# Kernel tuning notes

Measured on AMD Instinct MI355X. Metric: run time of the kernel, lower is better.

## Reference

```python
import jax, jax.numpy as jnp
import numpy as np

DIM = 192
HEADS = 6
WS = 7          # window size
SS = 3          # shift size
MLP_H = int(DIM * 4.0)
EPS_LN = 1e-5


def _static_tables():
    # Swin-v2 log-spaced continuous relative coords table: (1, 2*WS-1, 2*WS-1, 2)
    ch = np.arange(-(WS - 1), WS, dtype=np.float32)
    cw = np.arange(-(WS - 1), WS, dtype=np.float32)
    t = np.stack(np.meshgrid(ch, cw, indexing='ij'), axis=-1)[None]
    t[..., 0] /= (WS - 1)
    t[..., 1] /= (WS - 1)
    t *= 7.0
    t = np.sign(t) * np.log2(np.abs(t) + 1.0) / np.log2(7.0)
    # relative position index: (WS*WS, WS*WS)
    coords = np.stack(np.meshgrid(np.arange(WS), np.arange(WS), indexing='ij'))
    cf = coords.reshape(2, -1)
    rc = (cf[:, :, None] - cf[:, None, :]).transpose(1, 2, 0)
    rc[..., 0] += WS - 1
    rc[..., 1] += WS - 1
    rc[..., 0] *= 2 * WS - 1
    rpi = rc.sum(-1)
    return jnp.asarray(t, jnp.float32), jnp.asarray(rpi, jnp.int32)


def _attn_mask(H, W):
    # shifted-window mask: (nW, N, N) with 0 / -100
    img = np.zeros((H, W), np.float32)
    cnt = 0
    for hs in (slice(0, -WS), slice(-WS, -SS), slice(-SS, None)):
        for ws in (slice(0, -WS), slice(-WS, -SS), slice(-SS, None)):
            img[hs, ws] = cnt
            cnt += 1
    mw = img.reshape(H // WS, WS, W // WS, WS).transpose(0, 2, 1, 3).reshape(-1, WS * WS)
    am = mw[:, None, :] - mw[:, :, None]
    am = np.where(am != 0, -100.0, 0.0).astype(np.float32)
    return jnp.asarray(am)


def _ln(x, w, b):
    m = x.mean(-1, keepdims=True)
    v = ((x - m) ** 2).mean(-1, keepdims=True)
    return (x - m) / jnp.sqrt(v + EPS_LN) * w + b


def setup_inputs() -> dict:
    key = jax.random.key(0)
    ks = jax.random.split(key, 16)
    d = DIM
    inp = {
        'x': jax.random.normal(ks[0], (32, 56, 56, d), jnp.float32),
        'qkv_w': jax.random.normal(ks[1], (3 * d, d), jnp.float32) * (2.0 / d) ** 0.5,
        'qkv_b': jnp.full((3 * d,), 0.01, jnp.float32),
        'proj_w': jax.random.normal(ks[2], (d, d), jnp.float32) * (2.0 / d) ** 0.5,
        'proj_b': jnp.full((d,), 0.01, jnp.float32),
        'logit_scale': jnp.log(10.0 * jnp.ones((HEADS, 1, 1), jnp.float32)),
        'cpb_w1': jax.random.normal(ks[3], (512, 2), jnp.float32) * (2.0 / 2) ** 0.5,
        'cpb_b1': jnp.full((512,), 0.01, jnp.float32),
        'cpb_w2': jax.random.normal(ks[4], (HEADS, 512), jnp.float32) * (2.0 / 512) ** 0.5,
        'norm1_w': jnp.ones((d,), jnp.float32),
        'norm1_b': jnp.zeros((d,), jnp.float32),
        'norm2_w': jnp.ones((d,), jnp.float32),
        'norm2_b': jnp.zeros((d,), jnp.float32),
        'fc1_w': jax.random.normal(ks[5], (MLP_H, d), jnp.float32) * (2.0 / d) ** 0.5,
        'fc1_b': jnp.full((MLP_H,), 0.01, jnp.float32),
        'fc2_w': jax.random.normal(ks[6], (d, MLP_H), jnp.float32) * (2.0 / MLP_H) ** 0.5,
        'fc2_b': jnp.full((d,), 0.01, jnp.float32),
    }
    return inp


def reference(x, qkv_w, qkv_b, proj_w, proj_b, logit_scale, cpb_w1, cpb_b1, cpb_w2,
              norm1_w, norm1_b, norm2_w, norm2_b, fc1_w, fc1_b, fc2_w, fc2_b):
    B, H, W, C = x.shape
    N = WS * WS
    hd = C // HEADS
    table, rpi = _static_tables()
    mask = _attn_mask(H, W)  # (nW, N, N)
    nW = mask.shape[0]

    shortcut = x
    # cyclic shift + window partition: (B*nW, N, C)
    xs = jnp.roll(x, (-SS, -SS), axis=(1, 2))
    xw = xs.reshape(B, H // WS, WS, W // WS, WS, C).transpose(0, 1, 3, 2, 4, 5).reshape(-1, N, C)

    qkv = xw @ qkv_w.T + qkv_b
    qkv = qkv.reshape(-1, N, 3, HEADS, hd).transpose(2, 0, 3, 1, 4)
    q, k, v = qkv[0], qkv[1], qkv[2]  # (B_, H, N, hd)

    qn = q / jnp.clip(jnp.linalg.norm(q, axis=-1, keepdims=True), 1e-12)
    kn = k / jnp.clip(jnp.linalg.norm(k, axis=-1, keepdims=True), 1e-12)
    scale = jnp.exp(jnp.minimum(logit_scale, jnp.log(100.0)))  # (HEADS,1,1)
    attn = jnp.einsum('bhnd,bhmd->bhnm', qn, kn) * scale

    # CPB-MLP relative position bias
    hbt = jax.nn.leaky_relu(table @ cpb_w1.T + cpb_b1, 0.01) @ cpb_w2.T  # (1,13,13,HEADS)
    bias_table = hbt.reshape(-1, HEADS)
    rpb = bias_table[rpi.reshape(-1)].reshape(N, N, HEADS).transpose(2, 0, 1)
    attn = attn + (14.0 * jax.nn.sigmoid(rpb))[None]

    # shifted-window mask + softmax
    attn = attn.reshape(B, nW, HEADS, N, N) + mask[None, :, None]
    attn = jax.nn.softmax(attn.reshape(-1, HEADS, N, N), axis=-1)

    out = jnp.einsum('bhnm,bhmd->bnhd', attn, v).reshape(-1, N, C)
    out = out @ proj_w.T + proj_b

    # window reverse + reverse shift
    out = out.reshape(B, H // WS, W // WS, WS, WS, C).transpose(0, 1, 3, 2, 4, 5).reshape(B, H, W, C)
    out = jnp.roll(out, (SS, SS), axis=(1, 2))

    # post-norm residuals (Swin-v2 style)
    x1 = shortcut + _ln(out, norm1_w, norm1_b)
    mlp = jax.nn.gelu(x1 @ fc1_w.T + fc1_b, approximate=False) @ fc2_w.T + fc2_b
    return x1 + _ln(mlp, norm2_w, norm2_b)
```

## Files before the change

kernel.cpp:

```cpp
#include <hip/hip_runtime.h>
#include <math.h>

#define CDIM 192
#define NHEADS 6
#define HDIM 32
#define WSZ 7
#define NTOK 49
#define SHIFT 3
#define HW 56
#define MLPH 768
#define NTOKENS 100352
#define QKS 576
#define XS 200
#define VTS 72
#define PPS 72
#define LS 196
#define QPS 72
#define AS2 200
#define HS2 200
#define OS2 196

typedef __attribute__((ext_vector_type(8))) short short8;
typedef __attribute__((ext_vector_type(4))) float floatx4;
typedef unsigned short ushort_t;
typedef unsigned int uint_t;

__device__ __forceinline__ ushort_t f2b(float f) {
  __bf16 b = (__bf16)f;
  return __builtin_bit_cast(ushort_t, b);
}

__device__ __forceinline__ float gelu_fast(float v) {
  float u2 = 1.5957691f * v * (1.0f + 0.044715f * v * v);
  float s = 1.0f / (1.0f + __expf(-u2));
  return v * s;
}

__global__ void prep_kernel(const float* __restrict__ fc1_w, const float* __restrict__ fc2_w,
                            const float* __restrict__ qkv_w, const float* __restrict__ proj_w,
                            ushort_t* __restrict__ w1b, ushort_t* __restrict__ w2b,
                            ushort_t* __restrict__ qwb, ushort_t* __restrict__ pwb) {
  int i = blockIdx.x * 256 + threadIdx.x;
  if (i < MLPH*CDIM) w1b[i] = f2b(fc1_w[i]);
  else if (i < 2*MLPH*CDIM) w2b[i - MLPH*CDIM] = f2b(fc2_w[i - MLPH*CDIM]);
  else if (i < 2*MLPH*CDIM + 3*CDIM*CDIM) qwb[i - 2*MLPH*CDIM] = f2b(qkv_w[i - 2*MLPH*CDIM]);
  else if (i < 2*MLPH*CDIM + 4*CDIM*CDIM) {
    int j = i - 2*MLPH*CDIM - 3*CDIM*CDIM;
    int n = j / CDIM, k = j % CDIM;
    int h = k / 32, kloc = k % 32;
    int pos = (kloc < 16) ? 2*kloc : 2*(kloc-16) + 1;
    pwb[n*CDIM + h*32 + pos] = f2b(proj_w[j]);
  }
}

__global__ __launch_bounds__(256) void cpb1_kernel(const float* __restrict__ w1,
                                                   const float* __restrict__ b1,
                                                   const float* __restrict__ w2,
                                                   float* __restrict__ bt) {
  int wave = threadIdx.x >> 6, lane = threadIdx.x & 63;
  int e = blockIdx.x * 4 + wave;
  if (e >= 169) return;
  const float inv_log2_7 = 0.35620718710802217f;
  int a = e / 13, b = e % 13;
  float v0 = (float)(a - 6) * (7.0f / 6.0f);
  float v1 = (float)(b - 6) * (7.0f / 6.0f);
  float s0 = (v0 > 0.f) ? 1.f : ((v0 < 0.f) ? -1.f : 0.f);
  float s1 = (v1 > 0.f) ? 1.f : ((v1 < 0.f) ? -1.f : 0.f);
  v0 = s0 * log2f(fabsf(v0) + 1.0f) * inv_log2_7;
  v1 = s1 * log2f(fabsf(v1) + 1.0f) * inv_log2_7;
  float acc[NHEADS];
  #pragma unroll
  for (int h = 0; h < NHEADS; ++h) acc[h] = 0.f;
  #pragma unroll
  for (int j = 0; j < 8; ++j) {
    int k = lane + 64*j;
    float hv = v0 * w1[2*k] + v1 * w1[2*k+1] + b1[k];
    hv = (hv > 0.f) ? hv : 0.01f * hv;
    #pragma unroll
    for (int h = 0; h < NHEADS; ++h) acc[h] += hv * w2[h*512 + k];
  }
  #pragma unroll
  for (int m = 1; m < 64; m <<= 1)
    #pragma unroll
    for (int h = 0; h < NHEADS; ++h) acc[h] += __shfl_xor(acc[h], m, 64);
  if (lane == 0) {
    #pragma unroll
    for (int h = 0; h < NHEADS; ++h) bt[e*NHEADS + h] = acc[h];
  }
}

__global__ void cpb2_kernel(const float* __restrict__ bt, float* __restrict__ cbias) {
  int e = blockIdx.x * 256 + threadIdx.x;
  if (e >= 4*NHEADS*NTOK*NTOK) return;
  int cls = e / (NHEADS*NTOK*NTOK);
  int rem = e % (NHEADS*NTOK*NTOK);
  int h = rem / (NTOK*NTOK);
  int r = rem % (NTOK*NTOK);
  int i = r / NTOK, j = r % NTOK;
  int idx = (i/7 - j/7 + 6) * 13 + (i%7 - j%7 + 6);
  float v = bt[idx*NHEADS + h];
  float b = 14.0f / (1.0f + __expf(-v));
  int clsh = cls >> 1, clsw = cls & 1;
  int ri = (clsh ? HW-WSZ : 0) + i/7, rj = (clsh ? HW-WSZ : 0) + j/7;
  int ci = (clsw ? HW-WSZ : 0) + i%7, cj = (clsw ? HW-WSZ : 0) + j%7;
  int hi = (ri < HW-WSZ) ? 0 : ((ri < HW-SHIFT) ? 1 : 2);
  int hj = (rj < HW-WSZ) ? 0 : ((rj < HW-SHIFT) ? 1 : 2);
  int wi = (ci < HW-WSZ) ? 0 : ((ci < HW-SHIFT) ? 1 : 2);
  int wj = (cj < HW-WSZ) ? 0 : ((cj < HW-SHIFT) ? 1 : 2);
  if ((hi*3 + wi) != (hj*3 + wj)) b -= 100.f;
  cbias[e] = b;
}

__global__ __launch_bounds__(384) void qkv_kernel(
    const float* __restrict__ x, const ushort_t* __restrict__ qwb,
    const float* __restrict__ qkv_b, ushort_t* __restrict__ qkvg) {
  __shared__ __align__(16) ushort_t s_a[64*AS2];
  int tid = threadIdx.x;
  int lane = tid & 63;
  int h = tid >> 6;
  int l15 = lane & 15, quad = lane >> 4;
  size_t tbase = (size_t)blockIdx.x * 64;

  for (int e = tid; e < 64*48; e += 384) {
    int t = e / 48, cc = (e % 48) * 4;
    float4 v = *(const float4*)(x + (tbase + t)*CDIM + cc);
    uint_t p0 = (uint_t)f2b(v.x) | ((uint_t)f2b(v.y) << 16);
    uint_t p1 = (uint_t)f2b(v.z) | ((uint_t)f2b(v.w) << 16);
    *(uint_t*)&s_a[t*AS2 + cc]     = p0;
    *(uint_t*)&s_a[t*AS2 + cc + 2] = p1;
  }
  __syncthreads();

  floatx4 acc[6][4];
  #pragma unroll
  for (int nt = 0; nt < 6; ++nt)
    #pragma unroll
    for (int mt = 0; mt < 4; ++mt) acc[nt][mt] = (floatx4){0.f,0.f,0.f,0.f};
  #pragma unroll
  for (int kt = 0; kt < 6; ++kt) {
    short8 a[4];
    #pragma unroll
    for (int mt = 0; mt < 4; ++mt)
      a[mt] = *(const short8*)&s_a[(mt*16 + l15)*AS2 + kt*32 + quad*8];
    #pragma unroll
    for (int nt = 0; nt < 6; ++nt) {
      int o = (nt >> 1)*CDIM + h*HDIM + (nt & 1)*16 + l15;
      short8 b = *(const short8*)&qwb[(size_t)o*CDIM + kt*32 + quad*8];
      #pragma unroll
      for (int mt = 0; mt < 4; ++mt)
        acc[nt][mt] = __builtin_amdgcn_mfma_f32_16x16x32_bf16(a[mt], b, acc[nt][mt], 0, 0, 0);
    }
  }
  #pragma unroll
  for (int w2 = 0; w2 < 2; ++w2) {
    float b0 = qkv_b[w2*CDIM + h*HDIM + l15];
    float b1 = qkv_b[w2*CDIM + h*HDIM + 16 + l15];
    #pragma unroll
    for (int mt = 0; mt < 4; ++mt) {
      float vv[2][4], ss[4];
      #pragma unroll
      for (int r = 0; r < 4; ++r) {
        float t0 = acc[w2*2][mt][r] + b0;
        float t1 = acc[w2*2+1][mt][r] + b1;
        vv[0][r] = t0; vv[1][r] = t1;
        ss[r] = t0*t0 + t1*t1;
      }
      #pragma unroll
      for (int m = 1; m < 16; m <<= 1)
        #pragma unroll
        for (int r = 0; r < 4; ++r) ss[r] += __shfl_xor(ss[r], m, 64);
      #pragma unroll
      for (int r = 0; r < 4; ++r) {
        float inv = 1.0f / fmaxf(sqrtf(ss[r]), 1e-12f);
        size_t tok = tbase + mt*16 + quad*4 + r;
        uint_t pk = (uint_t)f2b(vv[0][r] * inv) | ((uint_t)f2b(vv[1][r] * inv) << 16);
        *(uint_t*)&qkvg[tok*QKS + w2*CDIM + h*HDIM + 2*l15] = pk;
      }
    }
  }
  {
    float b0 = qkv_b[2*CDIM + h*HDIM + l15];
    float b1 = qkv_b[2*CDIM + h*HDIM + 16 + l15];
    #pragma unroll
    for (int mt = 0; mt < 4; ++mt)
      #pragma unroll
      for (int r = 0; r < 4; ++r) {
        size_t tok = tbase + mt*16 + quad*4 + r;
        uint_t pk = (uint_t)f2b(acc[4][mt][r] + b0) | ((uint_t)f2b(acc[5][mt][r] + b1) << 16);
        *(uint_t*)&qkvg[tok*QKS + 2*CDIM + h*HDIM + 2*l15] = pk;
      }
  }
}

__global__ __launch_bounds__(512, 4) void attn_kernel(
    const float* __restrict__ x, const ushort_t* __restrict__ qkvg,
    const ushort_t* __restrict__ pwb, const float* __restrict__ proj_b,
    const float* __restrict__ logit_scale, const float* __restrict__ cbias,
    const float* __restrict__ n1w, const float* __restrict__ n1b,
    float* __restrict__ outp) {
  __shared__ __align__(16) ushort_t sm[192*VTS + 128*PPS + 64*XS];
  ushort_t* s_vt = sm;
  ushort_t* s_P  = sm + 192*VTS;
  ushort_t* s_o  = s_P + 128*PPS;
  float*    s_ln = (float*)sm;
  __shared__ float s_mu[NTOK], s_rs[NTOK];

  int tid = threadIdx.x;
  int lane = tid & 63;
  int wave = tid >> 6;
  int wm = wave & 3, wh = wave >> 2;
  int l15 = lane & 15, quad = lane >> 4;
  int mrow0 = wm*16 + quad*4;
  int blk = blockIdx.x;
  int bimg = blk >> 6, wh_b = (blk >> 3) & 7, ww_b = blk & 7;
  int rbase = wh_b*WSZ, cbase = ww_b*WSZ;
  const float* cb = cbias +
      (size_t)(((wh_b == 7) ? 2 : 0) + ((ww_b == 7) ? 1 : 0)) * (NHEADS*NTOK*NTOK);

  int ti_a = wm*16 + l15; ti_a = (ti_a < NTOK) ? ti_a : (NTOK-1);
  int ra = rbase + ti_a/7 + SHIFT; ra -= (ra >= HW) ? HW : 0;
  int ca = cbase + ti_a%7 + SHIFT; ca -= (ca >= HW) ? HW : 0;
  uint_t qrow = (uint_t)((bimg*HW + ra)*HW + ca) * QKS;
  uint_t krow[4];
  #pragma unroll
  for (int nt = 0; nt < 4; ++nt) {
    int tn = nt*16 + l15; tn = (tn < NTOK) ? tn : (NTOK-1);
    int r = rbase + tn/7 + SHIFT; r -= (r >= HW) ? HW : 0;
    int c = cbase + tn%7 + SHIFT; c -= (c >= HW) ? HW : 0;
    krow[nt] = (uint_t)((bimg*HW + r)*HW + c) * QKS + CDIM;
  }
  short8 aq[3];
  #pragma unroll
  for (int hh = 0; hh < 3; ++hh)
    aq[hh] = *(const short8*)&qkvg[(size_t)qrow + (wh*3+hh)*HDIM + quad*8];

  for (int e = tid; e < 32*48; e += 512) {
    int tp = e & 31, dg = e >> 5;
    int t0 = 2*tp, t1 = t0 + 1;
    uint2 va = make_uint2(0u, 0u), vb = make_uint2(0u, 0u);
    if (t0 < NTOK) {
      int r = rbase + t0/7 + SHIFT; r -= (r >= HW) ? HW : 0;
      int c = cbase + t0%7 + SHIFT; c -= (c >= HW) ? HW : 0;
      va = *(const uint2*)&qkvg[((size_t)((bimg*HW + r)*HW + c))*QKS + 2*CDIM + dg*4];
    }
    if (t1 < NTOK) {
      int r = rbase + t1/7 + SHIFT; r -= (r >= HW) ? HW : 0;
      int c = cbase + t1%7 + SHIFT; c -= (c >= HW) ? HW : 0;
      vb = *(const uint2*)&qkvg[((size_t)((bimg*HW + r)*HW + c))*QKS + 2*CDIM + dg*4];
    }
    int d = dg*4;
    *(uint_t*)&s_vt[(d  )*VTS + t0] = (va.x & 0xFFFFu) | (vb.x << 16);
    *(uint_t*)&s_vt[(d+1)*VTS + t0] = (va.x >> 16) | (vb.x & 0xFFFF0000u);
    *(uint_t*)&s_vt[(d+2)*VTS + t0] = (va.y & 0xFFFFu) | (vb.y << 16);
    *(uint_t*)&s_vt[(d+3)*VTS + t0] = (va.y >> 16) | (vb.y & 0xFFFF0000u);
  }
  __syncthreads();

  ushort_t* sPh = s_P + wave*16*PPS;
  short8 bk[4];
  #pragma unroll
  for (int nt = 0; nt < 4; ++nt)
    bk[nt] = *(const short8*)&qkvg[(size_t)krow[nt] + (wh*3)*HDIM + quad*8];
  for (int hh = 0; hh < 3; ++hh) {
    int h = wh*3 + hh;
    floatx4 sv[4];
    __builtin_amdgcn_s_setprio(1);
    #pragma unroll
    for (int nt = 0; nt < 4; ++nt)
      sv[nt] = __builtin_amdgcn_mfma_f32_16x16x32_bf16(aq[hh], bk[nt], (floatx4){0.f,0.f,0.f,0.f}, 0, 0, 0);
    __builtin_amdgcn_s_setprio(0);
    if (hh < 2) {
      #pragma unroll
      for (int nt = 0; nt < 4; ++nt)
        bk[nt] = *(const short8*)&qkvg[(size_t)krow[nt] + (h+1)*HDIM + quad*8];
    }
    float sc = __expf(fminf(logit_scale[h], 4.6051702f));
    #pragma unroll
    for (int r = 0; r < 4; ++r) {
      int m_tok = mrow0 + r;
      int mi = (m_tok < NTOK) ? m_tok : (NTOK-1);
      float srow[4];
      float mx = -1e30f;
      #pragma unroll
      for (int nt = 0; nt < 4; ++nt) {
        int n = nt*16 + l15;
        int ni = (n < NTOK) ? n : (NTOK-1);
        float s = sv[nt][r]*sc + cb[(h*NTOK + mi)*NTOK + ni];
        if (n >= NTOK) s = -1e30f;
        srow[nt] = s;
        mx = fmaxf(mx, s);
      }
      #pragma unroll
      for (int m = 1; m < 16; m <<= 1) mx = fmaxf(mx, __shfl_xor(mx, m, 64));
      float p[4], sum = 0.f;
      #pragma unroll
      for (int nt = 0; nt < 4; ++nt) { p[nt] = __expf(srow[nt] - mx); sum += p[nt]; }
      #pragma unroll
      for (int m = 1; m < 16; m <<= 1) sum += __shfl_xor(sum, m, 64);
      float inv = 1.0f / sum;
      #pragma unroll
      for (int nt = 0; nt < 4; ++nt) {
        int n = nt*16 + l15;
        sPh[(quad*4 + r)*PPS + n] = (n < NTOK) ? f2b(p[nt]*inv) : (ushort_t)0;
      }
    }
    floatx4 ov[2];
    ov[0] = (floatx4){0.f,0.f,0.f,0.f}; ov[1] = (floatx4){0.f,0.f,0.f,0.f};
    __builtin_amdgcn_s_setprio(1);
    #pragma unroll
    for (int kt = 0; kt < 2; ++kt) {
      short8 ap = *(const short8*)&sPh[l15*PPS + kt*32 + quad*8];
      #pragma unroll
      for (int dt = 0; dt < 2; ++dt) {
        short8 bv = *(const short8*)&s_vt[(h*HDIM + dt*16 + l15)*VTS + kt*32 + quad*8];
        ov[dt] = __builtin_amdgcn_mfma_f32_16x16x32_bf16(ap, bv, ov[dt], 0, 0, 0);
      }
    }
    __builtin_amdgcn_s_setprio(0);
    #pragma unroll
    for (int dt = 0; dt < 2; ++dt)
      #pragma unroll
      for (int r = 0; r < 4; ++r)
        s_o[(mrow0 + r)*XS + h*HDIM + dt*16 + l15] = f2b(ov[dt][r]);
  }
  __syncthreads();

  short8 aof[6];
  #pragma unroll
  for (int kt = 0; kt < 6; ++kt)
    aof[kt] = *(const short8*)&s_o[(wm*16 + l15)*XS + kt*32 + quad*8];
  floatx4 pacc[6];
  #pragma unroll
  for (int j = 0; j < 6; ++j) pacc[j] = (floatx4){0.f,0.f,0.f,0.f};
  #pragma unroll
  for (int kt = 0; kt < 6; ++kt) {
    #pragma unroll
    for (int j = 0; j < 6; ++j) {
      int n = wh*96 + j*16 + l15;
      short8 b = *(const short8*)&pwb[(size_t)n*CDIM + kt*32 + quad*8];
      pacc[j] = __builtin_amdgcn_mfma_f32_16x16x32_bf16(aof[kt], b, pacc[j], 0, 0, 0);
    }
  }
  #pragma unroll
  for (int j = 0; j < 6; ++j) {
    int c = wh*96 + j*16 + l15;
    float pb = proj_b[c];
    #pragma unroll
    for (int r = 0; r < 4; ++r) {
      int m = mrow0 + r;
      if (m < NTOK) s_ln[m*LS + c] = pacc[j][r] + pb;
    }
  }
  __syncthreads();
  if (tid < 4*NTOK) {
    int row = tid >> 2, part = tid & 3;
    const float4* rp = (const float4*)(s_ln + row*LS) + part*12;
    float mu = 0.f;
    #pragma unroll
    for (int c = 0; c < 12; ++c) { float4 v = rp[c]; mu += v.x+v.y+v.z+v.w; }
    mu += __shfl_xor(mu, 1, 64);
    mu += __shfl_xor(mu, 2, 64);
    mu *= (1.0f/CDIM);
    float var = 0.f;
    #pragma unroll
    for (int c = 0; c < 12; ++c) {
      float4 v = rp[c];
      float a0=v.x-mu, a1=v.y-mu, a2=v.z-mu, a3=v.w-mu;
      var += a0*a0 + a1*a1 + a2*a2 + a3*a3;
    }
    var += __shfl_xor(var, 1, 64);
    var += __shfl_xor(var, 2, 64);
    var *= (1.0f/CDIM);
    if (part == 0) { s_mu[row] = mu; s_rs[row] = rsqrtf(var + 1e-5f); }
  }
  __syncthreads();
  for (int e = tid; e < NTOK*48; e += 512) {
    int ti = e / 48, cc = (e % 48) * 4;
    int r = (rbase + ti/WSZ + SHIFT) % HW;
    int cl = (cbase + ti%WSZ + SHIFT) % HW;
    size_t g = (((size_t)bimg*HW + r)*HW + cl)*CDIM + cc;
    float4 xv = *(const float4*)(x + g);
    float4 wv = *(const float4*)(n1w + cc);
    float4 bv = *(const float4*)(n1b + cc);
    float mu = s_mu[ti], rs = s_rs[ti];
    float4 o;
    o.x = xv.x + (s_ln[ti*LS+cc  ] - mu)*rs*wv.x + bv.x;
    o.y = xv.y + (s_ln[ti*LS+cc+1] - mu)*rs*wv.y + bv.y;
    o.z = xv.z + (s_ln[ti*LS+cc+2] - mu)*rs*wv.z + bv.z;
    o.w = xv.w + (s_ln[ti*LS+cc+3] - mu)*rs*wv.w + bv.w;
    *(float4*)(outp + g) = o;
  }
}

__global__ __launch_bounds__(512, 4) void attn_fused(
    const float* __restrict__ x, const ushort_t* __restrict__ qwb,
    const float* __restrict__ qkv_b, const ushort_t* __restrict__ pwb,
    const float* __restrict__ proj_b, const float* __restrict__ logit_scale,
    const float* __restrict__ cbias, const float* __restrict__ n1w,
    const float* __restrict__ n1b, float* __restrict__ outp) {
  __shared__ __align__(16) ushort_t sm[64*XS + 2*64*QPS + 64*VTS + 2*64*PPS];
  ushort_t* s_x  = sm;
  ushort_t* s_qn = s_x  + 64*XS;
  ushort_t* s_kn = s_qn + 64*QPS;
  ushort_t* s_vt = s_kn + 64*QPS;
  ushort_t* s_P  = s_vt + 64*VTS;
  ushort_t* s_o  = s_x;
  float*    s_ln = (float*)sm;
  __shared__ float s_mu[NTOK], s_rs[NTOK];

  int tid = threadIdx.x;
  int lane = tid & 63;
  int wave = tid >> 6;
  int wm = wave & 3, wh = wave >> 2;
  int l15 = lane & 15, quad = lane >> 4;
  int mrow0 = wm*16 + quad*4;
  int blk = blockIdx.x;
  int bimg = blk >> 6, wh_b = (blk >> 3) & 7, ww_b = blk & 7;
  const float* cb = cbias +
      (size_t)(((wh_b == 7) ? 2 : 0) + ((ww_b == 7) ? 1 : 0)) * (NHEADS*NTOK*NTOK);

  for (int e = tid; e < 64*48; e += 512) {
    int i = e / 48, cc = (e % 48) * 4;
    uint_t p0 = 0, p1 = 0;
    if (i < NTOK) {
      int r = (wh_b*WSZ + i/WSZ + SHIFT) % HW;
      int c = (ww_b*WSZ + i%WSZ + SHIFT) % HW;
      float4 v = *(const float4*)(x + (((size_t)bimg*HW + r)*HW + c)*CDIM + cc);
      p0 = (uint_t)f2b(v.x) | ((uint_t)f2b(v.y) << 16);
      p1 = (uint_t)f2b(v.z) | ((uint_t)f2b(v.w) << 16);
    }
    *(uint_t*)&s_x[i*XS + cc]     = p0;
    *(uint_t*)&s_x[i*XS + cc + 2] = p1;
  }
  __syncthreads();

  short8 axf[6];
  #pragma unroll
  for (int kt = 0; kt < 6; ++kt)
    axf[kt] = *(const short8*)&s_x[(wm*16 + l15)*XS + kt*32 + quad*8];

  for (int g = 0; g < 3; ++g) {
    int h = g*2 + wh;
    floatx4 acc[6];
    #pragma unroll
    for (int nt = 0; nt < 6; ++nt) acc[nt] = (floatx4){0.f,0.f,0.f,0.f};
    #pragma unroll
    for (int kt = 0; kt < 6; ++kt) {
      short8 a = axf[kt];
      #pragma unroll
      for (int nt = 0; nt < 6; ++nt) {
        int o = (nt >> 1)*CDIM + h*HDIM + (nt & 1)*16 + l15;
        short8 b = *(const short8*)&qwb[(size_t)o*CDIM + kt*32 + quad*8];
        acc[nt] = __builtin_amdgcn_mfma_f32_16x16x32_bf16(a, b, acc[nt], 0, 0, 0);
      }
    }
    #pragma unroll
    for (int w2 = 0; w2 < 2; ++w2) {
      float vv[2][4], ss[4];
      #pragma unroll
      for (int r = 0; r < 4; ++r) ss[r] = 0.f;
      #pragma unroll
      for (int dt = 0; dt < 2; ++dt) {
        float bias = qkv_b[w2*CDIM + h*HDIM + dt*16 + l15];
        #pragma unroll
        for (int r = 0; r < 4; ++r) {
          float t = acc[w2*2 + dt][r] + bias;
          vv[dt][r] = t; ss[r] += t*t;
        }
      }
      #pragma unroll
      for (int m = 1; m < 16; m <<= 1)
        #pragma unroll
        for (int r = 0; r < 4; ++r) ss[r] += __shfl_xor(ss[r], m, 64);
      ushort_t* dst = w2 ? s_kn : s_qn;
      #pragma unroll
      for (int r = 0; r < 4; ++r) {
        float inv = 1.0f / fmaxf(sqrtf(ss[r]), 1e-12f);
        #pragma unroll
        for (int dt = 0; dt < 2; ++dt)
          dst[(mrow0 + r)*QPS + wh*HDIM + dt*16 + l15] = f2b(vv[dt][r] * inv);
      }
    }
    #pragma unroll
    for (int dt = 0; dt < 2; ++dt) {
      float bias = qkv_b[2*CDIM + h*HDIM + dt*16 + l15];
      int d = wh*HDIM + 2*l15 + dt;
      #pragma unroll
      for (int rp = 0; rp < 2; ++rp) {
        uint_t pk = (uint_t)f2b(acc[4+dt][2*rp] + bias) |
                    ((uint_t)f2b(acc[4+dt][2*rp+1] + bias) << 16);
        *(uint_t*)&s_vt[d*VTS + mrow0 + 2*rp] = pk;
      }
    }
    __syncthreads();

    short8 aq = *(const short8*)&s_qn[(wm*16 + l15)*QPS + wh*HDIM + quad*8];
    floatx4 sv[4];
    #pragma unroll
    for (int nt = 0; nt < 4; ++nt) {
      short8 bk = *(const short8*)&s_kn[(nt*16 + l15)*QPS + wh*HDIM + quad*8];
      sv[nt] = __builtin_amdgcn_mfma_f32_16x16x32_bf16(aq, bk, (floatx4){0.f,0.f,0.f,0.f}, 0, 0, 0);
    }
    float sc = __expf(fminf(logit_scale[h], 4.6051702f));
    ushort_t* sPh = s_P + wh*64*PPS;
    #pragma unroll
    for (int r = 0; r < 4; ++r) {
      int m_tok = mrow0 + r;
      int mi = (m_tok < NTOK) ? m_tok : (NTOK-1);
      float srow[4];
      float mx = -1e30f;
      #pragma unroll
      for (int nt = 0; nt < 4; ++nt) {
        int n = nt*16 + l15;
        int ni = (n < NTOK) ? n : (NTOK-1);
        float s = sv[nt][r]*sc + cb[(h*NTOK + mi)*NTOK + ni];
        if (n >= NTOK) s = -1e30f;
        srow[nt] = s;
        mx = fmaxf(mx, s);
      }
      #pragma unroll
      for (int m = 1; m < 16; m <<= 1) mx = fmaxf(mx, __shfl_xor(mx, m, 64));
      float p[4], sum = 0.f;
      #pragma unroll
      for (int nt = 0; nt < 4; ++nt) { p[nt] = __expf(srow[nt] - mx); sum += p[nt]; }
      #pragma unroll
      for (int m = 1; m < 16; m <<= 1) sum += __shfl_xor(sum, m, 64);
      float inv = 1.0f / sum;
      #pragma unroll
      for (int nt = 0; nt < 4; ++nt) {
        int n = nt*16 + l15;
        sPh[(mrow0 + r)*PPS + n] = (n < NTOK) ? f2b(p[nt]*inv) : (ushort_t)0;
      }
    }
    floatx4 ov[2];
    ov[0] = (floatx4){0.f,0.f,0.f,0.f}; ov[1] = (floatx4){0.f,0.f,0.f,0.f};
    #pragma unroll
    for (int kt = 0; kt < 2; ++kt) {
      short8 ap = *(const short8*)&sPh[(wm*16 + l15)*PPS + kt*32 + quad*8];
      #pragma unroll
      for (int dt = 0; dt < 2; ++dt) {
        short8 bv = *(const short8*)&s_vt[(wh*HDIM + dt*16 + l15)*VTS + kt*32 + quad*8];
        ov[dt] = __builtin_amdgcn_mfma_f32_16x16x32_bf16(ap, bv, ov[dt], 0, 0, 0);
      }
    }
    #pragma unroll
    for (int dt = 0; dt < 2; ++dt)
      #pragma unroll
      for (int r = 0; r < 4; ++r)
        s_o[(mrow0 + r)*XS + h*HDIM + dt*16 + l15] = f2b(ov[dt][r]);
    __syncthreads();
  }

  short8 aof[6];
  #pragma unroll
  for (int kt = 0; kt < 6; ++kt)
    aof[kt] = *(const short8*)&s_o[(wm*16 + l15)*XS + kt*32 + quad*8];
  __syncthreads();
  floatx4 pacc[6];
  #pragma unroll
  for (int j = 0; j < 6; ++j) pacc[j] = (floatx4){0.f,0.f,0.f,0.f};
  #pragma unroll
  for (int kt = 0; kt < 6; ++kt) {
    #pragma unroll
    for (int j = 0; j < 6; ++j) {
      int n = wh*96 + j*16 + l15;
      short8 b = *(const short8*)&pwb[(size_t)n*CDIM + kt*32 + quad*8];
      pacc[j] = __builtin_amdgcn_mfma_f32_16x16x32_bf16(aof[kt], b, pacc[j], 0, 0, 0);
    }
  }
  #pragma unroll
  for (int j = 0; j < 6; ++j) {
    int c = wh*96 + j*16 + l15;
    float pb = proj_b[c];
    #pragma unroll
    for (int r = 0; r < 4; ++r) {
      int m = mrow0 + r;
      if (m < NTOK) s_ln[m*LS + c] = pacc[j][r] + pb;
    }
  }
  __syncthreads();
  if (tid < NTOK) {
    const float4* row = (const float4*)(s_ln + tid*LS);
    float mu = 0.f;
    #pragma unroll 8
    for (int c = 0; c < 48; ++c) { float4 v = row[c]; mu += v.x+v.y+v.z+v.w; }
    mu *= (1.0f/CDIM);
    float var = 0.f;
    #pragma unroll 8
    for (int c = 0; c < 48; ++c) {
      float4 v = row[c];
      float a0=v.x-mu, a1=v.y-mu, a2=v.z-mu, a3=v.w-mu;
      var += a0*a0 + a1*a1 + a2*a2 + a3*a3;
    }
    var *= (1.0f/CDIM);
    s_mu[tid] = mu; s_rs[tid] = rsqrtf(var + 1e-5f);
  }
  __syncthreads();
  for (int e = tid; e < NTOK*48; e += 512) {
    int ti = e / 48, cc = (e % 48) * 4;
    int r = (wh_b*WSZ + ti/WSZ + SHIFT) % HW;
    int cl = (ww_b*WSZ + ti%WSZ + SHIFT) % HW;
    size_t g = (((size_t)bimg*HW + r)*HW + cl)*CDIM + cc;
    float4 xv = *(const float4*)(x + g);
    float4 wv = *(const float4*)(n1w + cc);
    float4 bv = *(const float4*)(n1b + cc);
    float mu = s_mu[ti], rs = s_rs[ti];
    float4 o;
    o.x = xv.x + (s_ln[ti*LS+cc  ] - mu)*rs*wv.x + bv.x;
    o.y = xv.y + (s_ln[ti*LS+cc+1] - mu)*rs*wv.y + bv.y;
    o.z = xv.z + (s_ln[ti*LS+cc+2] - mu)*rs*wv.z + bv.z;
    o.w = xv.w + (s_ln[ti*LS+cc+3] - mu)*rs*wv.w + bv.w;
    *(float4*)(outp + g) = o;
  }
}

__global__ __launch_bounds__(256) void mlp_kernel(
    const ushort_t* __restrict__ w1b, const ushort_t* __restrict__ w2b,
    const float* __restrict__ fc1_b, const float* __restrict__ fc2_b,
    const float* __restrict__ n2w, const float* __restrict__ n2b,
    float* __restrict__ io) {
  __shared__ __align__(16) ushort_t sm2[64*AS2 + 2*64*HS2];
  ushort_t* s_a  = sm2;
  ushort_t* s_h0 = sm2 + 64*AS2;
  ushort_t* s_h1 = s_h0 + 64*HS2;
  float*    s_o  = (float*)sm2;
  __shared__ float s_mu[64], s_rs[64];

  int tid = threadIdx.x;
  int lane = tid & 63;
  int wave = tid >> 6;
  int l15 = lane & 15, quad = lane >> 4;
  size_t base = (size_t)blockIdx.x * (64*CDIM);

  for (int e = tid; e < 64*48; e += 256) {
    int t = e / 48, cc = (e % 48) * 4;
    float4 v = *(const float4*)(io + base + t*CDIM + cc);
    uint_t p0 = (uint_t)f2b(v.x) | ((uint_t)f2b(v.y) << 16);
    uint_t p1 = (uint_t)f2b(v.z) | ((uint_t)f2b(v.w) << 16);
    *(uint_t*)&s_a[t*AS2 + cc]     = p0;
    *(uint_t*)&s_a[t*AS2 + cc + 2] = p1;
  }
  __syncthreads();

  floatx4 oacc[12];
  #pragma unroll
  for (int t = 0; t < 12; ++t) oacc[t] = (floatx4){0.f,0.f,0.f,0.f};

  #pragma unroll
  for (int ch = 0; ch < 4; ++ch) {
    ushort_t* sh = (ch & 1) ? s_h1 : s_h0;
    floatx4 hacc[12];
    #pragma unroll
    for (int t = 0; t < 12; ++t) hacc[t] = (floatx4){0.f,0.f,0.f,0.f};
    #pragma unroll
    for (int kt = 0; kt < 6; ++kt) {
      short8 a[4];
      #pragma unroll
      for (int mt = 0; mt < 4; ++mt)
        a[mt] = *(const short8*)&s_a[(mt*16 + l15)*AS2 + kt*32 + quad*8];
      #pragma unroll
      for (int nt = 0; nt < 3; ++nt) {
        int n = ch*192 + wave*48 + nt*16 + l15;
        short8 b = *(const short8*)&w1b[(size_t)n*CDIM + kt*32 + quad*8];
        #pragma unroll
        for (int mt = 0; mt < 4; ++mt)
          hacc[nt*4+mt] = __builtin_amdgcn_mfma_f32_16x16x32_bf16(a[mt], b, hacc[nt*4+mt], 0, 0, 0);
      }
    }
    #pragma unroll
    for (int nt = 0; nt < 3; ++nt) {
      int n = ch*192 + wave*48 + nt*16 + l15;
      int cloc = wave*48 + nt*16 + l15;
      float bias = fc1_b[n];
      #pragma unroll
      for (int mt = 0; mt < 4; ++mt) {
        #pragma unroll
        for (int r = 0; r < 4; ++r) {
          float v = hacc[nt*4+mt][r] + bias;
          sh[(mt*16 + quad*4 + r)*HS2 + cloc] = f2b(gelu_fast(v));
        }
      }
    }
    __syncthreads();
    #pragma unroll
    for (int kt = 0; kt < 6; ++kt) {
      short8 a2[4];
      #pragma unroll
      for (int mt = 0; mt < 4; ++mt)
        a2[mt] = *(const short8*)&sh[(mt*16 + l15)*HS2 + kt*32 + quad*8];
      #pragma unroll
      for (int nt = 0; nt < 3; ++nt) {
        int n2 = wave*48 + nt*16 + l15;
        short8 b2 = *(const short8*)&w2b[(size_t)n2*MLPH + ch*192 + kt*32 + quad*8];
        #pragma unroll
        for (int mt = 0; mt < 4; ++mt)
          oacc[nt*4+mt] = __builtin_amdgcn_mfma_f32_16x16x32_bf16(a2[mt], b2, oacc[nt*4+mt], 0, 0, 0);
      }
    }
  }

  #pragma unroll
  for (int nt = 0; nt < 3; ++nt) {
    int c = wave*48 + nt*16 + l15;
    float bb = fc2_b[c];
    #pragma unroll
    for (int mt = 0; mt < 4; ++mt) {
      #pragma unroll
      for (int r = 0; r < 4; ++r)
        s_o[(mt*16 + quad*4 + r)*OS2 + c] = oacc[nt*4+mt][r] + bb;
    }
  }
  __syncthreads();
  {
    int row = tid >> 2, part = tid & 3;
    const float4* rp = (const float4*)(s_o + row*OS2) + part*12;
    float mu = 0.f;
    #pragma unroll
    for (int c = 0; c < 12; ++c) { float4 v = rp[c]; mu += v.x+v.y+v.z+v.w; }
    mu += __shfl_xor(mu, 1, 64);
    mu += __shfl_xor(mu, 2, 64);
    mu *= (1.0f/CDIM);
    float var = 0.f;
    #pragma unroll
    for (int c = 0; c < 12; ++c) {
      float4 v = rp[c];
      float a0=v.x-mu, a1=v.y-mu, a2=v.z-mu, a3=v.w-mu;
      var += a0*a0 + a1*a1 + a2*a2 + a3*a3;
    }
    var += __shfl_xor(var, 1, 64);
    var += __shfl_xor(var, 2, 64);
    var *= (1.0f/CDIM);
    if (part == 0) { s_mu[row] = mu; s_rs[row] = rsqrtf(var + 1e-5f); }
  }
  __syncthreads();
  for (int e = tid; e < 64*48; e += 256) {
    int t = e / 48, cc = (e % 48) * 4;
    float4 xv = *(const float4*)(io + base + t*CDIM + cc);
    float4 wv = *(const float4*)(n2w + cc);
    float4 bv = *(const float4*)(n2b + cc);
    float mu = s_mu[t], rs = s_rs[t];
    float4 o;
    o.x = xv.x + (s_o[t*OS2+cc  ] - mu)*rs*wv.x + bv.x;
    o.y = xv.y + (s_o[t*OS2+cc+1] - mu)*rs*wv.y + bv.y;
    o.z = xv.z + (s_o[t*OS2+cc+2] - mu)*rs*wv.z + bv.z;
    o.w = xv.w + (s_o[t*OS2+cc+3] - mu)*rs*wv.w + bv.w;
    *(float4*)(io + base + t*CDIM + cc) = o;
  }
}

extern "C" void kernel_launch(void* const* d_in, const int* in_sizes, int n_in,
                              void* d_out, int out_size, void* d_ws, size_t ws_size,
                              hipStream_t stream) {
  const float* x           = (const float*)d_in[0];
  const float* qkv_w       = (const float*)d_in[1];
  const float* qkv_b       = (const float*)d_in[2];
  const float* proj_w      = (const float*)d_in[3];
  const float* proj_b      = (const float*)d_in[4];
  const float* logit_scale = (const float*)d_in[5];
  const float* cpb_w1      = (const float*)d_in[6];
  const float* cpb_b1      = (const float*)d_in[7];
  const float* cpb_w2      = (const float*)d_in[8];
  const float* n1w         = (const float*)d_in[9];
  const float* n1b         = (const float*)d_in[10];
  const float* n2w         = (const float*)d_in[11];
  const float* n2b         = (const float*)d_in[12];
  const float* fc1_w       = (const float*)d_in[13];
  const float* fc1_b       = (const float*)d_in[14];
  const float* fc2_w       = (const float*)d_in[15];
  const float* fc2_b       = (const float*)d_in[16];
  float* out = (float*)d_out;

  ushort_t* w1b = (ushort_t*)d_ws;
  ushort_t* w2b = w1b + MLPH*CDIM;
  ushort_t* qwb = w2b + CDIM*MLPH;
  ushort_t* pwb = qwb + 3*CDIM*CDIM;
  float* cbias  = (float*)(pwb + CDIM*CDIM);
  float* bt     = cbias + 4*NHEADS*NTOK*NTOK;
  ushort_t* qkvg = (ushort_t*)(bt + 169*NHEADS);

  size_t base_b = (size_t)(2*MLPH*CDIM + 4*CDIM*CDIM)*2
                + (size_t)(4*NHEADS*NTOK*NTOK)*4 + (size_t)(169*NHEADS)*4;
  size_t qkvg_b = (size_t)NTOKENS*QKS*2;
  bool split_qkv = ws_size >= base_b + qkvg_b;

  int prep_elems = 2*MLPH*CDIM + 4*CDIM*CDIM;
  hipLaunchKernelGGL(prep_kernel, dim3((prep_elems + 255)/256), dim3(256), 0, stream,
                     fc1_w, fc2_w, qkv_w, proj_w, w1b, w2b, qwb, pwb);
  hipLaunchKernelGGL(cpb1_kernel, dim3((169 + 3)/4), dim3(256), 0, stream,
                     cpb_w1, cpb_b1, cpb_w2, bt);
  hipLaunchKernelGGL(cpb2_kernel, dim3((4*NHEADS*NTOK*NTOK + 255)/256), dim3(256), 0, stream,
                     bt, cbias);
  if (split_qkv) {
    hipLaunchKernelGGL(qkv_kernel, dim3(NTOKENS/64), dim3(384), 0, stream,
                       x, qwb, qkv_b, qkvg);
    hipLaunchKernelGGL(attn_kernel, dim3(2048), dim3(512), 0, stream,
                       x, qkvg, pwb, proj_b, logit_scale, cbias, n1w, n1b, out);
  } else {
    hipLaunchKernelGGL(attn_fused, dim3(2048), dim3(512), 0, stream,
                       x, qwb, qkv_b, pwb, proj_b, logit_scale, cbias, n1w, n1b, out);
  }
  hipLaunchKernelGGL(mlp_kernel, dim3(NTOKENS/64), dim3(256), 0, stream,
                     w1b, w2b, fc1_b, fc2_b, n2w, n2b, out);
}
```

Before: 582.7 us.

## Split MLP kernel across 8 waves in 2x4 grid and vectorize V transpose load

```diff
diff --git a/kernel.cpp b/kernel.cpp
--- a/kernel.cpp
+++ b/kernel.cpp
@@ -234,25 +234,17 @@
   for (int hh = 0; hh < 3; ++hh)
     aq[hh] = *(const short8*)&qkvg[(size_t)qrow + (wh*3+hh)*HDIM + quad*8];
 
-  for (int e = tid; e < 32*48; e += 512) {
-    int tp = e & 31, dg = e >> 5;
-    int t0 = 2*tp, t1 = t0 + 1;
-    uint2 va = make_uint2(0u, 0u), vb = make_uint2(0u, 0u);
-    if (t0 < NTOK) {
-      int r = rbase + t0/7 + SHIFT; r -= (r >= HW) ? HW : 0;
-      int c = cbase + t0%7 + SHIFT; c -= (c >= HW) ? HW : 0;
-      va = *(const uint2*)&qkvg[((size_t)((bimg*HW + r)*HW + c))*QKS + 2*CDIM + dg*4];
-    }
-    if (t1 < NTOK) {
-      int r = rbase + t1/7 + SHIFT; r -= (r >= HW) ? HW : 0;
-      int c = cbase + t1%7 + SHIFT; c -= (c >= HW) ? HW : 0;
-      vb = *(const uint2*)&qkvg[((size_t)((bimg*HW + r)*HW + c))*QKS + 2*CDIM + dg*4];
-    }
-    int d = dg*4;
-    *(uint_t*)&s_vt[(d  )*VTS + t0] = (va.x & 0xFFFFu) | (vb.x << 16);
-    *(uint_t*)&s_vt[(d+1)*VTS + t0] = (va.x >> 16) | (vb.x & 0xFFFF0000u);
-    *(uint_t*)&s_vt[(d+2)*VTS + t0] = (va.y & 0xFFFFu) | (vb.y << 16);
-    *(uint_t*)&s_vt[(d+3)*VTS + t0] = (va.y >> 16) | (vb.y & 0xFFFF0000u);
+  for (int e = tid; e < 64*24; e += 512) {
+    int t = e / 24, cg = e % 24;
+    short8 v = (short8){0,0,0,0,0,0,0,0};
+    if (t < NTOK) {
+      int r = rbase + t/7 + SHIFT; r -= (r >= HW) ? HW : 0;
+      int c = cbase + t%7 + SHIFT; c -= (c >= HW) ? HW : 0;
+      v = *(const short8*)&qkvg[((size_t)((bimg*HW + r)*HW + c))*QKS + 2*CDIM + cg*8];
+    }
+    #pragma unroll
+    for (int j = 0; j < 8; ++j)
+      s_vt[(cg*8 + j)*VTS + t] = (ushort_t)v[j];
   }
   __syncthreads();
 
@@ -614,7 +606,7 @@
   }
 }
 
-__global__ __launch_bounds__(256) void mlp_kernel(
+__global__ __launch_bounds__(512, 4) void mlp_kernel(
     const ushort_t* __restrict__ w1b, const ushort_t* __restrict__ w2b,
     const float* __restrict__ fc1_b, const float* __restrict__ fc2_b,
     const float* __restrict__ n2w, const float* __restrict__ n2b,
@@ -629,10 +621,12 @@
   int tid = threadIdx.x;
   int lane = tid & 63;
   int wave = tid >> 6;
+  int wm = wave >> 2;
+  int wn = wave & 3;
   int l15 = lane & 15, quad = lane >> 4;
   size_t base = (size_t)blockIdx.x * (64*CDIM);
 
-  for (int e = tid; e < 64*48; e += 256) {
+  for (int e = tid; e < 64*48; e += 512) {
     int t = e / 48, cc = (e % 48) * 4;
     float4 v = *(const float4*)(io + base + t*CDIM + cc);
     uint_t p0 = (uint_t)f2b(v.x) | ((uint_t)f2b(v.y) << 16);
@@ -642,98 +636,100 @@
   }
   __syncthreads();
 
-  floatx4 oacc[12];
-  #pragma unroll
-  for (int t = 0; t < 12; ++t) oacc[t] = (floatx4){0.f,0.f,0.f,0.f};
+  floatx4 oacc[6];
+  #pragma unroll
+  for (int t = 0; t < 6; ++t) oacc[t] = (floatx4){0.f,0.f,0.f,0.f};
 
   #pragma unroll
   for (int ch = 0; ch < 4; ++ch) {
     ushort_t* sh = (ch & 1) ? s_h1 : s_h0;
-    floatx4 hacc[12];
-    #pragma unroll
-    for (int t = 0; t < 12; ++t) hacc[t] = (floatx4){0.f,0.f,0.f,0.f};
+    floatx4 hacc[6];
+    #pragma unroll
+    for (int t = 0; t < 6; ++t) hacc[t] = (floatx4){0.f,0.f,0.f,0.f};
     #pragma unroll
     for (int kt = 0; kt < 6; ++kt) {
-      short8 a[4];
-      #pragma unroll
-      for (int mt = 0; mt < 4; ++mt)
-        a[mt] = *(const short8*)&s_a[(mt*16 + l15)*AS2 + kt*32 + quad*8];
+      short8 a[2];
+      #pragma unroll
+      for (int mt = 0; mt < 2; ++mt)
+        a[mt] = *(const short8*)&s_a[(wm*32 + mt*16 + l15)*AS2 + kt*32 + quad*8];
       #pragma unroll
       for (int nt = 0; nt < 3; ++nt) {
-        int n = ch*192 + wave*48 + nt*16 + l15;
+        int n = ch*192 + wn*48 + nt*16 + l15;
         short8 b = *(const short8*)&w1b[(size_t)n*CDIM + kt*32 + quad*8];
         #pragma unroll
-        for (int mt = 0; mt < 4; ++mt)
-          hacc[nt*4+mt] = __builtin_amdgcn_mfma_f32_16x16x32_bf16(a[mt], b, hacc[nt*4+mt], 0, 0, 0);
+        for (int mt = 0; mt < 2; ++mt)
+          hacc[nt*2+mt] = __builtin_amdgcn_mfma_f32_16x16x32_bf16(a[mt], b, hacc[nt*2+mt], 0, 0, 0);
       }
     }
     #pragma unroll
     for (int nt = 0; nt < 3; ++nt) {
-      int n = ch*192 + wave*48 + nt*16 + l15;
-      int cloc = wave*48 + nt*16 + l15;
+      int n = ch*192 + wn*48 + nt*16 + l15;
+      int cloc = wn*48 + nt*16 + l15;
       float bias = fc1_b[n];
       #pragma unroll
-      for (int mt = 0; mt < 4; ++mt) {
+      for (int mt = 0; mt < 2; ++mt) {
         #pragma unroll
         for (int r = 0; r < 4; ++r) {
-          float v = hacc[nt*4+mt][r] + bias;
-          sh[(mt*16 + quad*4 + r)*HS2 + cloc] = f2b(gelu_fast(v));
+          float v = hacc[nt*2+mt][r] + bias;
+          sh[(wm*32 + mt*16 + quad*4 + r)*HS2 + cloc] = f2b(gelu_fast(v));
         }
       }
     }
     __syncthreads();
     #pragma unroll
     for (int kt = 0; kt < 6; ++kt) {
-      short8 a2[4];
-      #pragma unroll
-      for (int mt = 0; mt < 4; ++mt)
-        a2[mt] = *(const short8*)&sh[(mt*16 + l15)*HS2 + kt*32 + quad*8];
+      short8 a2[2];
+      #pragma unroll
+      for (int mt = 0; mt < 2; ++mt)
+        a2[mt] = *(const short8*)&sh[(wm*32 + mt*16 + l15)*HS2 + kt*32 + quad*8];
       #pragma unroll
       for (int nt = 0; nt < 3; ++nt) {
-        int n2 = wave*48 + nt*16 + l15;
+        int n2 = wn*48 + nt*16 + l15;
         short8 b2 = *(const short8*)&w2b[(size_t)n2*MLPH + ch*192 + kt*32 + quad*8];
         #pragma unroll
-        for (int mt = 0; mt < 4; ++mt)
-          oacc[nt*4+mt] = __builtin_amdgcn_mfma_f32_16x16x32_bf16(a2[mt], b2, oacc[nt*4+mt], 0, 0, 0);
+        for (int mt = 0; mt < 2; ++mt)
+          oacc[nt*2+mt] = __builtin_amdgcn_mfma_f32_16x16x32_bf16(a2[mt], b2, oacc[nt*2+mt], 0, 0, 0);
       }
     }
   }
 
   #pragma unroll
   for (int nt = 0; nt < 3; ++nt) {
-    int c = wave*48 + nt*16 + l15;
+    int c = wn*48 + nt*16 + l15;
     float bb = fc2_b[c];
     #pragma unroll
-    for (int mt = 0; mt < 4; ++mt) {
+    for (int mt = 0; mt < 2; ++mt) {
       #pragma unroll
       for (int r = 0; r < 4; ++r)
-        s_o[(mt*16 + quad*4 + r)*OS2 + c] = oacc[nt*4+mt][r] + bb;
+        s_o[(wm*32 + mt*16 + quad*4 + r)*OS2 + c] = oacc[nt*2+mt][r] + bb;
     }
   }
   __syncthreads();
   {
-    int row = tid >> 2, part = tid & 3;
-    const float4* rp = (const float4*)(s_o + row*OS2) + part*12;
+    int row = tid >> 3, part = tid & 7;
+    const float4* rp = (const float4*)(s_o + row*OS2) + part*6;
     float mu = 0.f;
     #pragma unroll
-    for (int c = 0; c < 12; ++c) { float4 v = rp[c]; mu += v.x+v.y+v.z+v.w; }
+    for (int c = 0; c < 6; ++c) { float4 v = rp[c]; mu += v.x+v.y+v.z+v.w; }
     mu += __shfl_xor(mu, 1, 64);
     mu += __shfl_xor(mu, 2, 64);
+    mu += __shfl_xor(mu, 4, 64);
     mu *= (1.0f/CDIM);
     float var = 0.f;
     #pragma unroll
-    for (int c = 0; c < 12; ++c) {
+    for (int c = 0; c < 6; ++c) {
       float4 v = rp[c];
       float a0=v.x-mu, a1=v.y-mu, a2=v.z-mu, a3=v.w-mu;
       var += a0*a0 + a1*a1 + a2*a2 + a3*a3;
     }
     var += __shfl_xor(var, 1, 64);
     var += __shfl_xor(var, 2, 64);
+    var += __shfl_xor(var, 4, 64);
     var *= (1.0f/CDIM);
     if (part == 0) { s_mu[row] = mu; s_rs[row] = rsqrtf(var + 1e-5f); }
   }
   __syncthreads();
-  for (int e = tid; e < 64*48; e += 256) {
+  for (int e = tid; e < 64*48; e += 512) {
     int t = e / 48, cc = (e % 48) * 4;
     float4 xv = *(const float4*)(io + base + t*CDIM + cc);
     float4 wv = *(const float4*)(n2w + cc);
@@ -799,6 +795,6 @@
     hipLaunchKernelGGL(attn_fused, dim3(2048), dim3(512), 0, stream,
                        x, qwb, qkv_b, pwb, proj_b, logit_scale, cbias, n1w, n1b, out);
   }
-  hipLaunchKernelGGL(mlp_kernel, dim3(NTOKENS/64), dim3(256), 0, stream,
+  hipLaunchKernelGGL(mlp_kernel, dim3(NTOKENS/64), dim3(512), 0, stream,
                      w1b, w2b, fc1_b, fc2_b, n2w, n2b, out);
 }
```

Result: slower. 683.0 us (+17.2%).
